# Kernel tuning notes

Hardware: AMD Instinct MI355X
Metric: run time of the kernel (lower is better)

Reference implementation:

```python
import jax, jax.numpy as jnp
import numpy as np

B, T, E, H = 2, 2048, 1024, 16
D = E // H  # head_size

def setup_inputs() -> dict:
    key = jax.random.key(0)
    ks = jax.random.split(key, 6)
    s = 0.02
    return {
        "x":  jax.random.normal(ks[0], (B, T, E), dtype=jnp.float32),
        "Wq": jax.random.normal(ks[1], (E, E), dtype=jnp.float32) * s,
        "Wk": jax.random.normal(ks[2], (E, E), dtype=jnp.float32) * s,
        "Wv": jax.random.normal(ks[3], (E, E), dtype=jnp.float32) * s,
        "Wp": jax.random.normal(ks[4], (E, E), dtype=jnp.float32) * s,
        "bp": jnp.zeros((E,), dtype=jnp.float32),
    }

def reference(x, Wq, Wk, Wv, Wp, bp):
    b, t, e = x.shape
    # Per-head Linear(E, D, bias=False) stacked == single [E,E] matmul then head split.
    # torch Linear: y = x @ W.T
    q = (x @ Wq.T).reshape(b, t, H, D).transpose(0, 2, 1, 3)  # (B,H,T,D)
    k = (x @ Wk.T).reshape(b, t, H, D).transpose(0, 2, 1, 3)
    v = (x @ Wv.T).reshape(b, t, H, D).transpose(0, 2, 1, 3)
    scale = jnp.asarray(D, x.dtype) ** -0.5
    wei = jnp.einsum('bhqd,bhkd->bhqk', q, k) * scale  # (B,H,T,T)
    causal = jnp.tril(jnp.ones((t, t), dtype=bool))
    wei = jnp.where(causal, wei, -jnp.inf)
    wei = jax.nn.softmax(wei, axis=-1)
    # dropout p=0.0 -> identity (eval-mode determinism)
    out = jnp.einsum('bhqk,bhkd->bhqd', wei, v)  # (B,H,T,D)
    out = out.transpose(0, 2, 1, 3).reshape(b, t, e)  # concat heads
    return out @ Wp.T + bp
```

## Files before the change

kernel.cpp:

```cpp
#include <hip/hip_runtime.h>

#define T_ 2048
#define E_ 1024
#define H_ 16
#define D_ 64
#define M_ 4096

typedef unsigned short ushort_t;
typedef __attribute__((ext_vector_type(8))) short bf16x8;
typedef __attribute__((ext_vector_type(4))) float f32x4;
typedef __attribute__((ext_vector_type(4))) unsigned short u16x4;
typedef __attribute__((ext_vector_type(8))) unsigned short u16x8;
typedef __attribute__((ext_vector_type(2))) unsigned int u32x2;

__device__ __forceinline__ ushort_t f2bf(float f) {
  union { float f; unsigned u; } v; v.f = f;
  unsigned r = v.u + 0x7FFFu + ((v.u >> 16) & 1u);
  return (ushort_t)(r >> 16);
}

__device__ __forceinline__ void gl16(const void* g, void* l) {
  __builtin_amdgcn_global_load_lds((const __attribute__((address_space(1))) void*)g,
                                   (__attribute__((address_space(3))) void*)l, 16, 0, 0);
}

__global__ __launch_bounds__(256)
void conv_all(const float* __restrict__ x,  const float* __restrict__ wq,
              const float* __restrict__ wk, const float* __restrict__ wv,
              const float* __restrict__ wp,
              ushort_t* __restrict__ xb,  ushort_t* __restrict__ wqb,
              ushort_t* __restrict__ wkb, ushort_t* __restrict__ wvb,
              ushort_t* __restrict__ wpb)
{
  const int id = blockIdx.x;
  const float* s; ushort_t* d; size_t off;
  if (id < 2048) { s = x; d = xb; off = (size_t)id * 2048; }
  else {
    int wsel = (id - 2048) >> 9, wid = (id - 2048) & 511;
    off = (size_t)wid * 2048;
    s = wsel == 0 ? wq : wsel == 1 ? wk : wsel == 2 ? wv : wp;
    d = wsel == 0 ? wqb : wsel == 1 ? wkb : wsel == 2 ? wvb : wpb;
  }
  size_t i = off + (size_t)threadIdx.x * 8;
  float4 a = *(const float4*)(s + i);
  float4 b = *(const float4*)(s + i + 4);
  u16x8 o;
  o[0]=f2bf(a.x); o[1]=f2bf(a.y); o[2]=f2bf(a.z); o[3]=f2bf(a.w);
  o[4]=f2bf(b.x); o[5]=f2bf(b.y); o[6]=f2bf(b.z); o[7]=f2bf(b.w);
  *(u16x8*)(d + i) = o;
}

__device__ __forceinline__ void gemm_core(const ushort_t* __restrict__ A,
                                          const ushort_t* __restrict__ W,
                                          int m0, int n0,
                                          ushort_t* As, ushort_t* Bs,
                                          f32x4 acc[4][4])
{
  const int t = threadIdx.x;
  const int lane = t & 63, w = t >> 6;
  const int g = lane >> 4, lq = lane & 15;
  const int wr = w >> 1, wc = w & 1;
  const int r0 = t >> 2;
  const int c0 = t & 3;
  const int ca0 = c0 ^ ((r0 >> 1) & 3);
  const int r1 = r0 + 64;
  const int ca1 = c0 ^ ((r1 >> 1) & 3);

  #pragma unroll
  for (int i = 0; i < 4; ++i)
    #pragma unroll
    for (int j = 0; j < 4; ++j) acc[i][j] = (f32x4){0.f,0.f,0.f,0.f};

  gl16(A + (size_t)(m0 + r0) * 1024 + ca0 * 8, As + t * 8);
  gl16(A + (size_t)(m0 + r1) * 1024 + ca1 * 8, As + 2048 + t * 8);
  gl16(W + (size_t)(n0 + r0) * 1024 + ca0 * 8, Bs + t * 8);
  gl16(W + (size_t)(n0 + r1) * 1024 + ca1 * 8, Bs + 2048 + t * 8);
  __syncthreads();

  int cur = 0;
  for (int k0 = 0; k0 < 1024; k0 += 32) {
    if (k0 + 32 < 1024) {
      const int nx = (cur ^ 1) * 4096;
      gl16(A + (size_t)(m0 + r0) * 1024 + k0 + 32 + ca0 * 8, As + nx + t * 8);
      gl16(A + (size_t)(m0 + r1) * 1024 + k0 + 32 + ca1 * 8, As + nx + 2048 + t * 8);
      gl16(W + (size_t)(n0 + r0) * 1024 + k0 + 32 + ca0 * 8, Bs + nx + t * 8);
      gl16(W + (size_t)(n0 + r1) * 1024 + k0 + 32 + ca1 * 8, Bs + nx + 2048 + t * 8);
    }
    const ushort_t* as = As + cur * 4096;
    const ushort_t* bs = Bs + cur * 4096;

    bf16x8 af[4], bfr[4];
    #pragma unroll
    for (int mi = 0; mi < 4; ++mi) {
      int row = wr * 64 + mi * 16 + lq;
      int ch = g ^ ((row >> 1) & 3);
      af[mi] = *(const bf16x8*)(as + row * 32 + ch * 8);
    }
    #pragma unroll
    for (int ni = 0; ni < 4; ++ni) {
      int row = wc * 64 + ni * 16 + lq;
      int ch = g ^ ((row >> 1) & 3);
      bfr[ni] = *(const bf16x8*)(bs + row * 32 + ch * 8);
    }
    __builtin_amdgcn_s_setprio(1);
    #pragma unroll
    for (int mi = 0; mi < 4; ++mi)
      #pragma unroll
      for (int ni = 0; ni < 4; ++ni)
        acc[mi][ni] = __builtin_amdgcn_mfma_f32_16x16x32_bf16(af[mi], bfr[ni], acc[mi][ni], 0, 0, 0);
    __builtin_amdgcn_s_setprio(0);

    __syncthreads();
    cur ^= 1;
  }
}

__global__ __launch_bounds__(256)
void gemm_qkv(const ushort_t* __restrict__ xb,
              const ushort_t* __restrict__ wqb, const ushort_t* __restrict__ wkb,
              const ushort_t* __restrict__ wvb,
              ushort_t* __restrict__ Qd, ushort_t* __restrict__ Kd, ushort_t* __restrict__ Vd)
{
  __shared__ __align__(16) ushort_t As[2 * 4096];
  __shared__ __align__(16) ushort_t Bs[2 * 4096];
  const int bx = blockIdx.x;
  const int sel = bx >> 3;
  const int n0 = (bx & 7) * 128;
  const int m0 = blockIdx.y * 128;
  const ushort_t* W = sel == 0 ? wqb : (sel == 1 ? wkb : wvb);
  f32x4 acc[4][4];
  gemm_core(xb, W, m0, n0, As, Bs, acc);

  const int t = threadIdx.x, lane = t & 63, w = t >> 6;
  const int g = lane >> 4, lq = lane & 15, wr = w >> 1, wc = w & 1;
  const float scl = (sel == 0) ? 0.125f : 1.0f;
  ushort_t* dst = sel == 0 ? Qd : (sel == 1 ? Kd : Vd);
  #pragma unroll
  for (int mi = 0; mi < 4; ++mi)
    #pragma unroll
    for (int ni = 0; ni < 4; ++ni)
      #pragma unroll
      for (int r = 0; r < 4; ++r) {
        int m = m0 + wr * 64 + mi * 16 + 4 * g + r;
        int n = n0 + wc * 64 + ni * 16 + lq;
        int b = m >> 11, tt = m & (T_ - 1);
        int h = n >> 6, d = n & (D_ - 1);
        ushort_t v = f2bf(acc[mi][ni][r] * scl);
        if (sel < 2) dst[((size_t)(b * H_ + h) * T_ + tt) * D_ + d] = v;
        else         dst[((size_t)(b * H_ + h) * D_ + d) * T_ + tt] = v;
      }
}

__global__ __launch_bounds__(256)
void gemm_out64(const ushort_t* __restrict__ Ab, const ushort_t* __restrict__ wpb,
                const float* __restrict__ bias, float* __restrict__ out)
{
  __shared__ __align__(16) ushort_t As[2 * 2048];
  __shared__ __align__(16) ushort_t Bs[2 * 4096];
  const int t = threadIdx.x, lane = t & 63, w = t >> 6;
  const int g = lane >> 4, lq = lane & 15;
  const int n0 = blockIdx.x * 128;
  const int m0 = blockIdx.y * 64;
  const int r0 = t >> 2, c0 = t & 3;
  const int ca0 = c0 ^ ((r0 >> 1) & 3);
  const int r1 = r0 + 64;
  const int ca1 = c0 ^ ((r1 >> 1) & 3);

  f32x4 acc[4][2];
  #pragma unroll
  for (int i = 0; i < 4; ++i) { acc[i][0] = (f32x4){0.f,0.f,0.f,0.f}; acc[i][1] = (f32x4){0.f,0.f,0.f,0.f}; }

  gl16(Ab  + (size_t)(m0 + r0) * 1024 + ca0 * 8, As + t * 8);
  gl16(wpb + (size_t)(n0 + r0) * 1024 + ca0 * 8, Bs + t * 8);
  gl16(wpb + (size_t)(n0 + r1) * 1024 + ca1 * 8, Bs + 2048 + t * 8);
  __syncthreads();

  int cur = 0;
  for (int k0 = 0; k0 < 1024; k0 += 32) {
    if (k0 + 32 < 1024) {
      gl16(Ab  + (size_t)(m0 + r0) * 1024 + k0 + 32 + ca0 * 8, As + (cur ^ 1) * 2048 + t * 8);
      gl16(wpb + (size_t)(n0 + r0) * 1024 + k0 + 32 + ca0 * 8, Bs + (cur ^ 1) * 4096 + t * 8);
      gl16(wpb + (size_t)(n0 + r1) * 1024 + k0 + 32 + ca1 * 8, Bs + (cur ^ 1) * 4096 + 2048 + t * 8);
    }
    const ushort_t* as = As + cur * 2048;
    const ushort_t* bs = Bs + cur * 4096;

    bf16x8 af[4], bfr[2];
    #pragma unroll
    for (int mi = 0; mi < 4; ++mi) {
      int row = mi * 16 + lq;
      int ch = g ^ ((row >> 1) & 3);
      af[mi] = *(const bf16x8*)(as + row * 32 + ch * 8);
    }
    #pragma unroll
    for (int ni = 0; ni < 2; ++ni) {
      int row = w * 32 + ni * 16 + lq;
      int ch = g ^ ((row >> 1) & 3);
      bfr[ni] = *(const bf16x8*)(bs + row * 32 + ch * 8);
    }
    __builtin_amdgcn_s_setprio(1);
    #pragma unroll
    for (int mi = 0; mi < 4; ++mi)
      #pragma unroll
      for (int ni = 0; ni < 2; ++ni)
        acc[mi][ni] = __builtin_amdgcn_mfma_f32_16x16x32_bf16(af[mi], bfr[ni], acc[mi][ni], 0, 0, 0);
    __builtin_amdgcn_s_setprio(0);

    __syncthreads();
    cur ^= 1;
  }
  #pragma unroll
  for (int mi = 0; mi < 4; ++mi)
    #pragma unroll
    for (int ni = 0; ni < 2; ++ni)
      #pragma unroll
      for (int r = 0; r < 4; ++r) {
        int m = m0 + mi * 16 + 4 * g + r;
        int n = n0 + w * 32 + ni * 16 + lq;
        out[(size_t)m * E_ + n] = acc[mi][ni][r] + bias[n];
      }
}

__global__ __launch_bounds__(256, 2)
void attn_mfma(const ushort_t* __restrict__ Q, const ushort_t* __restrict__ K,
               const ushort_t* __restrict__ Vt, ushort_t* __restrict__ O)
{
  __shared__ __align__(16) ushort_t Ps[128 * 72];
  const int t = threadIdx.x, w = t >> 6, lane = t & 63;
  const int g = lane >> 4, lq = lane & 15;
  const int i = blockIdx.x;
  const int xcd = i & 7, chunk = i >> 3;
  const int bh = xcd * 4 + (chunk >> 4);
  const int qt = (chunk < 32) ? (chunk & 15) : (15 - (chunk & 15));
  const int q0 = qt * 128;
  const size_t qkbase = (size_t)bh * T_ * D_;
  const size_t vbase  = (size_t)bh * D_ * T_;

  const int rowA = 32 * w + lq, rowB = rowA + 16;
  const int qgA = q0 + rowA, qgB = q0 + rowB;
  const bf16x8 qA0 = *(const bf16x8*)(Q + qkbase + (size_t)qgA * D_ + g * 8);
  const bf16x8 qA1 = *(const bf16x8*)(Q + qkbase + (size_t)qgA * D_ + 32 + g * 8);
  const bf16x8 qB0 = *(const bf16x8*)(Q + qkbase + (size_t)qgB * D_ + g * 8);
  const bf16x8 qB1 = *(const bf16x8*)(Q + qkbase + (size_t)qgB * D_ + 32 + g * 8);

  f32x4 accA[4], accB[4];
  #pragma unroll
  for (int db = 0; db < 4; ++db) { accA[db] = (f32x4){0.f,0.f,0.f,0.f}; accB[db] = (f32x4){0.f,0.f,0.f,0.f}; }
  float mA = -1e30f, lA = 0.f, mB = -1e30f, lB = 0.f;

  const int nt = 2 * qt + 2;

  for (int kt = 0; kt < nt; ++kt) {
    const int k0 = kt * 64;

    bf16x8 kf0[4], kf1[4], vf0[4], vf1[4];
    #pragma unroll
    for (int kb = 0; kb < 4; ++kb) {
      const ushort_t* kp = K + qkbase + (size_t)(k0 + kb * 16 + lq) * D_;
      kf0[kb] = *(const bf16x8*)(kp + g * 8);
      kf1[kb] = *(const bf16x8*)(kp + 32 + g * 8);
    }
    #pragma unroll
    for (int db = 0; db < 4; ++db) {
      const ushort_t* vp = Vt + vbase + (size_t)(db * 16 + lq) * T_ + k0;
      vf0[db] = *(const bf16x8*)(vp + g * 8);
      vf1[db] = *(const bf16x8*)(vp + 32 + g * 8);
    }

    f32x4 stA[4], stB[4];
    __builtin_amdgcn_s_setprio(1);
    #pragma unroll
    for (int kb = 0; kb < 4; ++kb) {
      f32x4 zA = (f32x4){0.f,0.f,0.f,0.f};
      zA = __builtin_amdgcn_mfma_f32_16x16x32_bf16(kf0[kb], qA0, zA, 0, 0, 0);
      zA = __builtin_amdgcn_mfma_f32_16x16x32_bf16(kf1[kb], qA1, zA, 0, 0, 0);
      stA[kb] = zA;
      f32x4 zB = (f32x4){0.f,0.f,0.f,0.f};
      zB = __builtin_amdgcn_mfma_f32_16x16x32_bf16(kf0[kb], qB0, zB, 0, 0, 0);
      zB = __builtin_amdgcn_mfma_f32_16x16x32_bf16(kf1[kb], qB1, zB, 0, 0, 0);
      stB[kb] = zB;
    }
    __builtin_amdgcn_s_setprio(0);

    if (kt >= nt - 2) {
      #pragma unroll
      for (int kb = 0; kb < 4; ++kb)
        #pragma unroll
        for (int r = 0; r < 4; ++r) {
          int kg = k0 + kb * 16 + 4 * g + r;
          if (kg > qgA) stA[kb][r] = -1e30f;
          if (kg > qgB) stB[kb][r] = -1e30f;
        }
    }

    float tmA = -1e30f, tmB = -1e30f;
    #pragma unroll
    for (int kb = 0; kb < 4; ++kb)
      #pragma unroll
      for (int r = 0; r < 4; ++r) { tmA = fmaxf(tmA, stA[kb][r]); tmB = fmaxf(tmB, stB[kb][r]); }
    tmA = fmaxf(tmA, __shfl_xor(tmA, 16)); tmA = fmaxf(tmA, __shfl_xor(tmA, 32));
    tmB = fmaxf(tmB, __shfl_xor(tmB, 16)); tmB = fmaxf(tmB, __shfl_xor(tmB, 32));

    if (!__all((tmA <= mA + 8.f) && (tmB <= mB + 8.f))) {
      float mnA = fmaxf(mA, tmA), mnB = fmaxf(mB, tmB);
      float alA = __expf(mA - mnA), alB = __expf(mB - mnB);
      mA = mnA; mB = mnB;
      lA *= alA; lB *= alB;
      float alAr[4], alBr[4];
      #pragma unroll
      for (int r = 0; r < 4; ++r) { alAr[r] = __shfl(alA, 4 * g + r); alBr[r] = __shfl(alB, 4 * g + r); }
      #pragma unroll
      for (int db = 0; db < 4; ++db)
        #pragma unroll
        for (int r = 0; r < 4; ++r) { accA[db][r] *= alAr[r]; accB[db][r] *= alBr[r]; }
    }

    float tsA = 0.f, tsB = 0.f;
    #pragma unroll
    for (int kb = 0; kb < 4; ++kb) {
      float pA0 = __expf(stA[kb][0] - mA), pA1 = __expf(stA[kb][1] - mA);
      float pA2 = __expf(stA[kb][2] - mA), pA3 = __expf(stA[kb][3] - mA);
      float pB0 = __expf(stB[kb][0] - mB), pB1 = __expf(stB[kb][1] - mB);
      float pB2 = __expf(stB[kb][2] - mB), pB3 = __expf(stB[kb][3] - mB);
      tsA += (pA0 + pA1) + (pA2 + pA3);
      tsB += (pB0 + pB1) + (pB2 + pB3);
      unsigned aLo, aHi, bLo, bHi;
      asm("v_cvt_pk_bf16_f32 %0, %1, %2" : "=v"(aLo) : "v"(pA0), "v"(pA1));
      asm("v_cvt_pk_bf16_f32 %0, %1, %2" : "=v"(aHi) : "v"(pA2), "v"(pA3));
      asm("v_cvt_pk_bf16_f32 %0, %1, %2" : "=v"(bLo) : "v"(pB0), "v"(pB1));
      asm("v_cvt_pk_bf16_f32 %0, %1, %2" : "=v"(bHi) : "v"(pB2), "v"(pB3));
      *(u32x2*)(Ps + rowA * 72 + kb * 16 + 4 * g) = (u32x2){aLo, aHi};
      *(u32x2*)(Ps + rowB * 72 + kb * 16 + 4 * g) = (u32x2){bLo, bHi};
    }
    tsA += __shfl_xor(tsA, 16); tsA += __shfl_xor(tsA, 32);
    tsB += __shfl_xor(tsB, 16); tsB += __shfl_xor(tsB, 32);
    lA += tsA; lB += tsB;

    asm volatile("s_waitcnt lgkmcnt(0)" ::: "memory");
    bf16x8 paA0 = *(const bf16x8*)(Ps + rowA * 72 + g * 8);
    bf16x8 paA1 = *(const bf16x8*)(Ps + rowA * 72 + 32 + g * 8);
    bf16x8 paB0 = *(const bf16x8*)(Ps + rowB * 72 + g * 8);
    bf16x8 paB1 = *(const bf16x8*)(Ps + rowB * 72 + 32 + g * 8);

    __builtin_amdgcn_s_setprio(1);
    #pragma unroll
    for (int db = 0; db < 4; ++db) {
      accA[db] = __builtin_amdgcn_mfma_f32_16x16x32_bf16(paA0, vf0[db], accA[db], 0, 0, 0);
      accA[db] = __builtin_amdgcn_mfma_f32_16x16x32_bf16(paA1, vf1[db], accA[db], 0, 0, 0);
      accB[db] = __builtin_amdgcn_mfma_f32_16x16x32_bf16(paB0, vf0[db], accB[db], 0, 0, 0);
      accB[db] = __builtin_amdgcn_mfma_f32_16x16x32_bf16(paB1, vf1[db], accB[db], 0, 0, 0);
    }
    __builtin_amdgcn_s_setprio(0);
  }

  float invA = 1.0f / lA, invB = 1.0f / lB;
  float liA[4], liB[4];
  #pragma unroll
  for (int r = 0; r < 4; ++r) { liA[r] = __shfl(invA, 4 * g + r); liB[r] = __shfl(invB, 4 * g + r); }
  const int b = bh >> 4, h = bh & 15;
  #pragma unroll
  for (int db = 0; db < 4; ++db)
    #pragma unroll
    for (int r = 0; r < 4; ++r) {
      int mAo = q0 + 32 * w + 4 * g + r;
      int mBo = mAo + 16;
      O[((size_t)(b * T_ + mAo)) * E_ + h * 64 + db * 16 + lq] = f2bf(accA[db][r] * liA[r]);
      O[((size_t)(b * T_ + mBo)) * E_ + h * 64 + db * 16 + lq] = f2bf(accB[db][r] * liB[r]);
    }
}

extern "C" void kernel_launch(void* const* d_in, const int* in_sizes, int n_in,
                              void* d_out, int out_size, void* d_ws, size_t ws_size,
                              hipStream_t stream) {
  const float* x  = (const float*)d_in[0];
  const float* Wq = (const float*)d_in[1];
  const float* Wk = (const float*)d_in[2];
  const float* Wv = (const float*)d_in[3];
  const float* Wp = (const float*)d_in[4];
  const float* bp = (const float*)d_in[5];
  float* out = (float*)d_out;

  ushort_t* ws  = (ushort_t*)d_ws;
  ushort_t* xb  = ws;
  ushort_t* wqb = xb  + (size_t)M_ * E_;
  ushort_t* wkb = wqb + (size_t)E_ * E_;
  ushort_t* wvb = wkb + (size_t)E_ * E_;
  ushort_t* wpb = wvb + (size_t)E_ * E_;
  ushort_t* Qb  = wpb + (size_t)E_ * E_;
  ushort_t* Kb  = Qb  + (size_t)M_ * E_;
  ushort_t* Vb  = Kb  + (size_t)M_ * E_;
  ushort_t* Ab  = Vb  + (size_t)M_ * E_;

  conv_all<<<4096, 256, 0, stream>>>(x, Wq, Wk, Wv, Wp, xb, wqb, wkb, wvb, wpb);
  gemm_qkv<<<dim3(24, 32), 256, 0, stream>>>(xb, wqb, wkb, wvb, Qb, Kb, Vb);
  attn_mfma<<<512, 256, 0, stream>>>(Qb, Kb, Vb, Ab);
  gemm_out64<<<dim3(8, 64), 256, 0, stream>>>(Ab, wpb, bp, out);
}
```

Measured before the change: 135.1 us.

## Software-pipeline K tile loads with double-buffered registers in attention loop

Unrolls the key-tile loop by two and double-buffers K fragments in registers, so the next tile's K is prefetched while the current tile's softmax and PV work run. V loads are issued after the QK MFMAs so they overlap the softmax arithmetic. The aim is to hide global load latency behind compute, at the cost of higher register pressure that could lower occupancy or cause spills.

```diff
diff --git a/kernel.cpp b/kernel.cpp
--- a/kernel.cpp
+++ b/kernel.cpp
@@ -9,7 +9,6 @@
 typedef unsigned short ushort_t;
 typedef __attribute__((ext_vector_type(8))) short bf16x8;
 typedef __attribute__((ext_vector_type(4))) float f32x4;
-typedef __attribute__((ext_vector_type(4))) unsigned short u16x4;
 typedef __attribute__((ext_vector_type(8))) unsigned short u16x8;
 typedef __attribute__((ext_vector_type(2))) unsigned int u32x2;
 
@@ -250,108 +249,129 @@
 
   const int nt = 2 * qt + 2;
 
-  for (int kt = 0; kt < nt; ++kt) {
-    const int k0 = kt * 64;
-
-    bf16x8 kf0[4], kf1[4], vf0[4], vf1[4];
-    #pragma unroll
-    for (int kb = 0; kb < 4; ++kb) {
-      const ushort_t* kp = K + qkbase + (size_t)(k0 + kb * 16 + lq) * D_;
-      kf0[kb] = *(const bf16x8*)(kp + g * 8);
-      kf1[kb] = *(const bf16x8*)(kp + 32 + g * 8);
-    }
-    #pragma unroll
-    for (int db = 0; db < 4; ++db) {
-      const ushort_t* vp = Vt + vbase + (size_t)(db * 16 + lq) * T_ + k0;
-      vf0[db] = *(const bf16x8*)(vp + g * 8);
-      vf1[db] = *(const bf16x8*)(vp + 32 + g * 8);
-    }
-
-    f32x4 stA[4], stB[4];
-    __builtin_amdgcn_s_setprio(1);
-    #pragma unroll
-    for (int kb = 0; kb < 4; ++kb) {
-      f32x4 zA = (f32x4){0.f,0.f,0.f,0.f};
-      zA = __builtin_amdgcn_mfma_f32_16x16x32_bf16(kf0[kb], qA0, zA, 0, 0, 0);
-      zA = __builtin_amdgcn_mfma_f32_16x16x32_bf16(kf1[kb], qA1, zA, 0, 0, 0);
-      stA[kb] = zA;
-      f32x4 zB = (f32x4){0.f,0.f,0.f,0.f};
-      zB = __builtin_amdgcn_mfma_f32_16x16x32_bf16(kf0[kb], qB0, zB, 0, 0, 0);
-      zB = __builtin_amdgcn_mfma_f32_16x16x32_bf16(kf1[kb], qB1, zB, 0, 0, 0);
-      stB[kb] = zB;
-    }
-    __builtin_amdgcn_s_setprio(0);
-
-    if (kt >= nt - 2) {
-      #pragma unroll
-      for (int kb = 0; kb < 4; ++kb)
-        #pragma unroll
-        for (int r = 0; r < 4; ++r) {
-          int kg = k0 + kb * 16 + 4 * g + r;
-          if (kg > qgA) stA[kb][r] = -1e30f;
-          if (kg > qgB) stB[kb][r] = -1e30f;
-        }
-    }
-
-    float tmA = -1e30f, tmB = -1e30f;
-    #pragma unroll
-    for (int kb = 0; kb < 4; ++kb)
-      #pragma unroll
-      for (int r = 0; r < 4; ++r) { tmA = fmaxf(tmA, stA[kb][r]); tmB = fmaxf(tmB, stB[kb][r]); }
-    tmA = fmaxf(tmA, __shfl_xor(tmA, 16)); tmA = fmaxf(tmA, __shfl_xor(tmA, 32));
-    tmB = fmaxf(tmB, __shfl_xor(tmB, 16)); tmB = fmaxf(tmB, __shfl_xor(tmB, 32));
-
-    if (!__all((tmA <= mA + 8.f) && (tmB <= mB + 8.f))) {
-      float mnA = fmaxf(mA, tmA), mnB = fmaxf(mB, tmB);
-      float alA = __expf(mA - mnA), alB = __expf(mB - mnB);
-      mA = mnA; mB = mnB;
-      lA *= alA; lB *= alB;
-      float alAr[4], alBr[4];
-      #pragma unroll
-      for (int r = 0; r < 4; ++r) { alAr[r] = __shfl(alA, 4 * g + r); alBr[r] = __shfl(alB, 4 * g + r); }
-      #pragma unroll
-      for (int db = 0; db < 4; ++db)
-        #pragma unroll
-        for (int r = 0; r < 4; ++r) { accA[db][r] *= alAr[r]; accB[db][r] *= alBr[r]; }
-    }
-
-    float tsA = 0.f, tsB = 0.f;
-    #pragma unroll
-    for (int kb = 0; kb < 4; ++kb) {
-      float pA0 = __expf(stA[kb][0] - mA), pA1 = __expf(stA[kb][1] - mA);
-      float pA2 = __expf(stA[kb][2] - mA), pA3 = __expf(stA[kb][3] - mA);
-      float pB0 = __expf(stB[kb][0] - mB), pB1 = __expf(stB[kb][1] - mB);
-      float pB2 = __expf(stB[kb][2] - mB), pB3 = __expf(stB[kb][3] - mB);
-      tsA += (pA0 + pA1) + (pA2 + pA3);
-      tsB += (pB0 + pB1) + (pB2 + pB3);
-      unsigned aLo, aHi, bLo, bHi;
-      asm("v_cvt_pk_bf16_f32 %0, %1, %2" : "=v"(aLo) : "v"(pA0), "v"(pA1));
-      asm("v_cvt_pk_bf16_f32 %0, %1, %2" : "=v"(aHi) : "v"(pA2), "v"(pA3));
-      asm("v_cvt_pk_bf16_f32 %0, %1, %2" : "=v"(bLo) : "v"(pB0), "v"(pB1));
-      asm("v_cvt_pk_bf16_f32 %0, %1, %2" : "=v"(bHi) : "v"(pB2), "v"(pB3));
-      *(u32x2*)(Ps + rowA * 72 + kb * 16 + 4 * g) = (u32x2){aLo, aHi};
-      *(u32x2*)(Ps + rowB * 72 + kb * 16 + 4 * g) = (u32x2){bLo, bHi};
-    }
-    tsA += __shfl_xor(tsA, 16); tsA += __shfl_xor(tsA, 32);
-    tsB += __shfl_xor(tsB, 16); tsB += __shfl_xor(tsB, 32);
-    lA += tsA; lB += tsB;
-
-    asm volatile("s_waitcnt lgkmcnt(0)" ::: "memory");
-    bf16x8 paA0 = *(const bf16x8*)(Ps + rowA * 72 + g * 8);
-    bf16x8 paA1 = *(const bf16x8*)(Ps + rowA * 72 + 32 + g * 8);
-    bf16x8 paB0 = *(const bf16x8*)(Ps + rowB * 72 + g * 8);
-    bf16x8 paB1 = *(const bf16x8*)(Ps + rowB * 72 + 32 + g * 8);
-
-    __builtin_amdgcn_s_setprio(1);
-    #pragma unroll
-    for (int db = 0; db < 4; ++db) {
-      accA[db] = __builtin_amdgcn_mfma_f32_16x16x32_bf16(paA0, vf0[db], accA[db], 0, 0, 0);
-      accA[db] = __builtin_amdgcn_mfma_f32_16x16x32_bf16(paA1, vf1[db], accA[db], 0, 0, 0);
-      accB[db] = __builtin_amdgcn_mfma_f32_16x16x32_bf16(paB0, vf0[db], accB[db], 0, 0, 0);
-      accB[db] = __builtin_amdgcn_mfma_f32_16x16x32_bf16(paB1, vf1[db], accB[db], 0, 0, 0);
-    }
-    __builtin_amdgcn_s_setprio(0);
+  bf16x8 kfa0[4], kfa1[4], kfb0[4], kfb1[4];
+  bf16x8 vf0[4], vf1[4];
+
+#define LOADK(K0_, KF0_, KF1_)                                                \
+  do {                                                                        \
+    _Pragma("unroll")                                                         \
+    for (int _i = 0; _i < 4; ++_i) {                                          \
+      const ushort_t* _kp = K + qkbase + (size_t)((K0_) + _i * 16 + lq) * D_; \
+      KF0_[_i] = *(const bf16x8*)(_kp + g * 8);                               \
+      KF1_[_i] = *(const bf16x8*)(_kp + 32 + g * 8);                          \
+    }                                                                         \
+  } while (0)
+
+#define LOADV(K0_)                                                              \
+  do {                                                                          \
+    _Pragma("unroll")                                                           \
+    for (int _i = 0; _i < 4; ++_i) {                                            \
+      const ushort_t* _vp = Vt + vbase + (size_t)(_i * 16 + lq) * T_ + (K0_);   \
+      vf0[_i] = *(const bf16x8*)(_vp + g * 8);                                  \
+      vf1[_i] = *(const bf16x8*)(_vp + 32 + g * 8);                             \
+    }                                                                           \
+  } while (0)
+
+#define STEP(K0_, KF0_, KF1_, KN0_, NKF0_, NKF1_, DOMASK)                       \
+  do {                                                                          \
+    const int _k0 = (K0_);                                                      \
+    f32x4 stA[4], stB[4];                                                       \
+    __builtin_amdgcn_s_setprio(1);                                              \
+    _Pragma("unroll")                                                           \
+    for (int _kb = 0; _kb < 4; ++_kb) {                                         \
+      f32x4 zA = (f32x4){0.f,0.f,0.f,0.f};                                      \
+      zA = __builtin_amdgcn_mfma_f32_16x16x32_bf16(KF0_[_kb], qA0, zA, 0, 0, 0);\
+      zA = __builtin_amdgcn_mfma_f32_16x16x32_bf16(KF1_[_kb], qA1, zA, 0, 0, 0);\
+      stA[_kb] = zA;                                                            \
+      f32x4 zB = (f32x4){0.f,0.f,0.f,0.f};                                      \
+      zB = __builtin_amdgcn_mfma_f32_16x16x32_bf16(KF0_[_kb], qB0, zB, 0, 0, 0);\
+      zB = __builtin_amdgcn_mfma_f32_16x16x32_bf16(KF1_[_kb], qB1, zB, 0, 0, 0);\
+      stB[_kb] = zB;                                                            \
+    }                                                                           \
+    __builtin_amdgcn_s_setprio(0);                                              \
+    LOADV(_k0);                          \
+    if ((KN0_) >= 0) LOADK((KN0_), NKF0_, NKF1_);          \
+    if (DOMASK) {                                                               \
+      _Pragma("unroll")                                                         \
+      for (int _kb = 0; _kb < 4; ++_kb)                                         \
+        _Pragma("unroll")                                                       \
+        for (int _r = 0; _r < 4; ++_r) {                                        \
+          int _kg = _k0 + _kb * 16 + 4 * g + _r;                                \
+          if (_kg > qgA) stA[_kb][_r] = -1e30f;                                 \
+          if (_kg > qgB) stB[_kb][_r] = -1e30f;                                 \
+        }                                                                       \
+    }                                                                           \
+    float tmA = -1e30f, tmB = -1e30f;                                           \
+    _Pragma("unroll")                                                           \
+    for (int _kb = 0; _kb < 4; ++_kb)                                           \
+      _Pragma("unroll")                                                         \
+      for (int _r = 0; _r < 4; ++_r) {                                          \
+        tmA = fmaxf(tmA, stA[_kb][_r]); tmB = fmaxf(tmB, stB[_kb][_r]);         \
+      }                                                                         \
+    tmA = fmaxf(tmA, __shfl_xor(tmA, 16)); tmA = fmaxf(tmA, __shfl_xor(tmA, 32));\
+    tmB = fmaxf(tmB, __shfl_xor(tmB, 16)); tmB = fmaxf(tmB, __shfl_xor(tmB, 32));\
+    if (!__all((tmA <= mA + 8.f) && (tmB <= mB + 8.f))) {                       \
+      float mnA = fmaxf(mA, tmA), mnB = fmaxf(mB, tmB);                         \
+      float alA = __expf(mA - mnA), alB = __expf(mB - mnB);                     \
+      mA = mnA; mB = mnB;                                                       \
+      lA *= alA; lB *= alB;                                                     \
+      float alAr[4], alBr[4];                                                   \
+      _Pragma("unroll")                                                         \
+      for (int _r = 0; _r < 4; ++_r) {                                          \
+        alAr[_r] = __shfl(alA, 4 * g + _r); alBr[_r] = __shfl(alB, 4 * g + _r); \
+      }                                                                         \
+      _Pragma("unroll")                                                         \
+      for (int _db = 0; _db < 4; ++_db)                                         \
+        _Pragma("unroll")                                                       \
+        for (int _r = 0; _r < 4; ++_r) {                                        \
+          accA[_db][_r] *= alAr[_r]; accB[_db][_r] *= alBr[_r];                 \
+        }                                                                       \
+    }                                                                           \
+    float tsA = 0.f, tsB = 0.f;                                                 \
+    _Pragma("unroll")                                                           \
+    for (int _kb = 0; _kb < 4; ++_kb) {                                         \
+      float pA0 = __expf(stA[_kb][0] - mA), pA1 = __expf(stA[_kb][1] - mA);     \
+      float pA2 = __expf(stA[_kb][2] - mA), pA3 = __expf(stA[_kb][3] - mA);     \
+      float pB0 = __expf(stB[_kb][0] - mB), pB1 = __expf(stB[_kb][1] - mB);     \
+      float pB2 = __expf(stB[_kb][2] - mB), pB3 = __expf(stB[_kb][3] - mB);     \
+      tsA += (pA0 + pA1) + (pA2 + pA3);                                         \
+      tsB += (pB0 + pB1) + (pB2 + pB3);                                         \
+      unsigned aLo, aHi, bLo, bHi;                                              \
+      asm("v_cvt_pk_bf16_f32 %0, %1, %2" : "=v"(aLo) : "v"(pA0), "v"(pA1));     \
+      asm("v_cvt_pk_bf16_f32 %0, %1, %2" : "=v"(aHi) : "v"(pA2), "v"(pA3));     \
+      asm("v_cvt_pk_bf16_f32 %0, %1, %2" : "=v"(bLo) : "v"(pB0), "v"(pB1));     \
+      asm("v_cvt_pk_bf16_f32 %0, %1, %2" : "=v"(bHi) : "v"(pB2), "v"(pB3));     \
+      *(u32x2*)(Ps + rowA * 72 + _kb * 16 + 4 * g) = (u32x2){aLo, aHi};         \
+      *(u32x2*)(Ps + rowB * 72 + _kb * 16 + 4 * g) = (u32x2){bLo, bHi};         \
+    }                                                                           \
+    tsA += __shfl_xor(tsA, 16); tsA += __shfl_xor(tsA, 32);                     \
+    tsB += __shfl_xor(tsB, 16); tsB += __shfl_xor(tsB, 32);                     \
+    lA += tsA; lB += tsB;                                                       \
+    asm volatile("s_waitcnt lgkmcnt(0)" ::: "memory");                          \
+    bf16x8 paA0 = *(const bf16x8*)(Ps + rowA * 72 + g * 8);                     \
+    bf16x8 paA1 = *(const bf16x8*)(Ps + rowA * 72 + 32 + g * 8);                \
+    bf16x8 paB0 = *(const bf16x8*)(Ps + rowB * 72 + g * 8);                     \
+    bf16x8 paB1 = *(const bf16x8*)(Ps + rowB * 72 + 32 + g * 8);                \
+    __builtin_amdgcn_s_setprio(1);                                              \
+    _Pragma("unroll")                                                           \
+    for (int _db = 0; _db < 4; ++_db) {                                         \
+      accA[_db] = __builtin_amdgcn_mfma_f32_16x16x32_bf16(paA0, vf0[_db], accA[_db], 0, 0, 0); \
+      accA[_db] = __builtin_amdgcn_mfma_f32_16x16x32_bf16(paA1, vf1[_db], accA[_db], 0, 0, 0); \
+      accB[_db] = __builtin_amdgcn_mfma_f32_16x16x32_bf16(paB0, vf0[_db], accB[_db], 0, 0, 0); \
+      accB[_db] = __builtin_amdgcn_mfma_f32_16x16x32_bf16(paB1, vf1[_db], accB[_db], 0, 0, 0); \
+    }                                                                           \
+    __builtin_amdgcn_s_setprio(0);                                              \
+  } while (0)
+
+  LOADK(0, kfa0, kfa1);
+  for (int kt = 0; kt < nt; kt += 2) {
+    const bool last = (kt == nt - 2);
+    STEP(kt * 64,       kfa0, kfa1, (kt + 1) * 64,                       kfb0, kfb1, last);
+    STEP((kt + 1) * 64, kfb0, kfb1, (kt + 2 < nt) ? (kt + 2) * 64 : -1,  kfa0, kfa1, last);
   }
+#undef LOADK
+#undef LOADV
+#undef STEP
 
   float invA = 1.0f / lA, invB = 1.0f / lB;
   float liA[4], liB[4];
```

After: 135.7 us. No clear change (+0.4%).

## Halve attention query tile to 64 rows and double grid with longest-first ordering

Applied to the files above, without the earlier changes.

The attention kernel now gives each block 64 query rows (one 16-row tile per wave) instead of 128 (two per wave), which doubles the grid to 1024 blocks and raises the launch-bounds occupancy hint to 4 blocks per CU. The block order changes from an XCD-aware swizzle with paired query tiles to a simple longest-first order across (batch, head). The intent is better load balance over the causal triangle, less register pressure and more waves in flight. In exchange each loaded K/V tile feeds half as many query rows, so global and L2 traffic for K and V roughly doubles, and the XCD cache locality of the old mapping is lost.

```diff
diff --git a/kernel.cpp b/kernel.cpp
--- a/kernel.cpp
+++ b/kernel.cpp
@@ -9,7 +9,6 @@
 typedef unsigned short ushort_t;
 typedef __attribute__((ext_vector_type(8))) short bf16x8;
 typedef __attribute__((ext_vector_type(4))) float f32x4;
-typedef __attribute__((ext_vector_type(4))) unsigned short u16x4;
 typedef __attribute__((ext_vector_type(8))) unsigned short u16x8;
 typedef __attribute__((ext_vector_type(2))) unsigned int u32x2;
 
@@ -221,34 +220,31 @@
       }
 }
 
-__global__ __launch_bounds__(256, 2)
+__global__ __launch_bounds__(256, 4)
 void attn_mfma(const ushort_t* __restrict__ Q, const ushort_t* __restrict__ K,
                const ushort_t* __restrict__ Vt, ushort_t* __restrict__ O)
 {
-  __shared__ __align__(16) ushort_t Ps[128 * 72];
+  __shared__ __align__(16) ushort_t Ps[64 * 72];
   const int t = threadIdx.x, w = t >> 6, lane = t & 63;
   const int g = lane >> 4, lq = lane & 15;
   const int i = blockIdx.x;
-  const int xcd = i & 7, chunk = i >> 3;
-  const int bh = xcd * 4 + (chunk >> 4);
-  const int qt = (chunk < 32) ? (chunk & 15) : (15 - (chunk & 15));
-  const int q0 = qt * 128;
+  const int qt = 31 - (i >> 5);
+  const int bh = i & 31;
+  const int q0 = qt * 64;
   const size_t qkbase = (size_t)bh * T_ * D_;
   const size_t vbase  = (size_t)bh * D_ * T_;
 
-  const int rowA = 32 * w + lq, rowB = rowA + 16;
-  const int qgA = q0 + rowA, qgB = q0 + rowB;
+  const int rowA = 16 * w + lq;
+  const int qgA = q0 + rowA;
   const bf16x8 qA0 = *(const bf16x8*)(Q + qkbase + (size_t)qgA * D_ + g * 8);
   const bf16x8 qA1 = *(const bf16x8*)(Q + qkbase + (size_t)qgA * D_ + 32 + g * 8);
-  const bf16x8 qB0 = *(const bf16x8*)(Q + qkbase + (size_t)qgB * D_ + g * 8);
-  const bf16x8 qB1 = *(const bf16x8*)(Q + qkbase + (size_t)qgB * D_ + 32 + g * 8);
-
-  f32x4 accA[4], accB[4];
-  #pragma unroll
-  for (int db = 0; db < 4; ++db) { accA[db] = (f32x4){0.f,0.f,0.f,0.f}; accB[db] = (f32x4){0.f,0.f,0.f,0.f}; }
-  float mA = -1e30f, lA = 0.f, mB = -1e30f, lB = 0.f;
-
-  const int nt = 2 * qt + 2;
+
+  f32x4 acc[4];
+  #pragma unroll
+  for (int db = 0; db < 4; ++db) acc[db] = (f32x4){0.f,0.f,0.f,0.f};
+  float mA = -1e30f, lA = 0.f;
+
+  const int nt = qt + 1;
 
   for (int kt = 0; kt < nt; ++kt) {
     const int k0 = kt * 64;
@@ -267,105 +263,88 @@
       vf1[db] = *(const bf16x8*)(vp + 32 + g * 8);
     }
 
-    f32x4 stA[4], stB[4];
+    f32x4 st[4];
     __builtin_amdgcn_s_setprio(1);
     #pragma unroll
     for (int kb = 0; kb < 4; ++kb) {
-      f32x4 zA = (f32x4){0.f,0.f,0.f,0.f};
-      zA = __builtin_amdgcn_mfma_f32_16x16x32_bf16(kf0[kb], qA0, zA, 0, 0, 0);
-      zA = __builtin_amdgcn_mfma_f32_16x16x32_bf16(kf1[kb], qA1, zA, 0, 0, 0);
-      stA[kb] = zA;
-      f32x4 zB = (f32x4){0.f,0.f,0.f,0.f};
-      zB = __builtin_amdgcn_mfma_f32_16x16x32_bf16(kf0[kb], qB0, zB, 0, 0, 0);
-      zB = __builtin_amdgcn_mfma_f32_16x16x32_bf16(kf1[kb], qB1, zB, 0, 0, 0);
-      stB[kb] = zB;
+      f32x4 z = (f32x4){0.f,0.f,0.f,0.f};
+      z = __builtin_amdgcn_mfma_f32_16x16x32_bf16(kf0[kb], qA0, z, 0, 0, 0);
+      z = __builtin_amdgcn_mfma_f32_16x16x32_bf16(kf1[kb], qA1, z, 0, 0, 0);
+      st[kb] = z;
     }
     __builtin_amdgcn_s_setprio(0);
 
-    if (kt >= nt - 2) {
+    if (kt == nt - 1) {
       #pragma unroll
       for (int kb = 0; kb < 4; ++kb)
         #pragma unroll
         for (int r = 0; r < 4; ++r) {
           int kg = k0 + kb * 16 + 4 * g + r;
-          if (kg > qgA) stA[kb][r] = -1e30f;
-          if (kg > qgB) stB[kb][r] = -1e30f;
+          if (kg > qgA) st[kb][r] = -1e30f;
         }
     }
 
-    float tmA = -1e30f, tmB = -1e30f;
+    float tm = -1e30f;
     #pragma unroll
     for (int kb = 0; kb < 4; ++kb)
       #pragma unroll
-      for (int r = 0; r < 4; ++r) { tmA = fmaxf(tmA, stA[kb][r]); tmB = fmaxf(tmB, stB[kb][r]); }
-    tmA = fmaxf(tmA, __shfl_xor(tmA, 16)); tmA = fmaxf(tmA, __shfl_xor(tmA, 32));
-    tmB = fmaxf(tmB, __shfl_xor(tmB, 16)); tmB = fmaxf(tmB, __shfl_xor(tmB, 32));
-
-    if (!__all((tmA <= mA + 8.f) && (tmB <= mB + 8.f))) {
-      float mnA = fmaxf(mA, tmA), mnB = fmaxf(mB, tmB);
-      float alA = __expf(mA - mnA), alB = __expf(mB - mnB);
-      mA = mnA; mB = mnB;
-      lA *= alA; lB *= alB;
-      float alAr[4], alBr[4];
-      #pragma unroll
-      for (int r = 0; r < 4; ++r) { alAr[r] = __shfl(alA, 4 * g + r); alBr[r] = __shfl(alB, 4 * g + r); }
+      for (int r = 0; r < 4; ++r) tm = fmaxf(tm, st[kb][r]);
+    tm = fmaxf(tm, __shfl_xor(tm, 16));
+    tm = fmaxf(tm, __shfl_xor(tm, 32));
+
+    if (!__all(tm <= mA + 8.f)) {
+      float mn = fmaxf(mA, tm);
+      float al = __expf(mA - mn);
+      mA = mn;
+      lA *= al;
+      float alr[4];
+      #pragma unroll
+      for (int r = 0; r < 4; ++r) alr[r] = __shfl(al, 4 * g + r);
       #pragma unroll
       for (int db = 0; db < 4; ++db)
         #pragma unroll
-        for (int r = 0; r < 4; ++r) { accA[db][r] *= alAr[r]; accB[db][r] *= alBr[r]; }
-    }
-
-    float tsA = 0.f, tsB = 0.f;
+        for (int r = 0; r < 4; ++r) acc[db][r] *= alr[r];
+    }
+
+    float ts = 0.f;
     #pragma unroll
     for (int kb = 0; kb < 4; ++kb) {
-      float pA0 = __expf(stA[kb][0] - mA), pA1 = __expf(stA[kb][1] - mA);
-      float pA2 = __expf(stA[kb][2] - mA), pA3 = __expf(stA[kb][3] - mA);
-      float pB0 = __expf(stB[kb][0] - mB), pB1 = __expf(stB[kb][1] - mB);
-      float pB2 = __expf(stB[kb][2] - mB), pB3 = __expf(stB[kb][3] - mB);
-      tsA += (pA0 + pA1) + (pA2 + pA3);
-      tsB += (pB0 + pB1) + (pB2 + pB3);
-      unsigned aLo, aHi, bLo, bHi;
-      asm("v_cvt_pk_bf16_f32 %0, %1, %2" : "=v"(aLo) : "v"(pA0), "v"(pA1));
-      asm("v_cvt_pk_bf16_f32 %0, %1, %2" : "=v"(aHi) : "v"(pA2), "v"(pA3));
-      asm("v_cvt_pk_bf16_f32 %0, %1, %2" : "=v"(bLo) : "v"(pB0), "v"(pB1));
-      asm("v_cvt_pk_bf16_f32 %0, %1, %2" : "=v"(bHi) : "v"(pB2), "v"(pB3));
-      *(u32x2*)(Ps + rowA * 72 + kb * 16 + 4 * g) = (u32x2){aLo, aHi};
-      *(u32x2*)(Ps + rowB * 72 + kb * 16 + 4 * g) = (u32x2){bLo, bHi};
-    }
-    tsA += __shfl_xor(tsA, 16); tsA += __shfl_xor(tsA, 32);
-    tsB += __shfl_xor(tsB, 16); tsB += __shfl_xor(tsB, 32);
-    lA += tsA; lB += tsB;
+      float p0 = __expf(st[kb][0] - mA), p1 = __expf(st[kb][1] - mA);
+      float p2 = __expf(st[kb][2] - mA), p3 = __expf(st[kb][3] - mA);
+      ts += (p0 + p1) + (p2 + p3);
+      unsigned lo, hi;
+      asm("v_cvt_pk_bf16_f32 %0, %1, %2" : "=v"(lo) : "v"(p0), "v"(p1));
+      asm("v_cvt_pk_bf16_f32 %0, %1, %2" : "=v"(hi) : "v"(p2), "v"(p3));
+      *(u32x2*)(Ps + rowA * 72 + kb * 16 + 4 * g) = (u32x2){lo, hi};
+    }
+    ts += __shfl_xor(ts, 16);
+    ts += __shfl_xor(ts, 32);
+    lA += ts;
 
     asm volatile("s_waitcnt lgkmcnt(0)" ::: "memory");
-    bf16x8 paA0 = *(const bf16x8*)(Ps + rowA * 72 + g * 8);
-    bf16x8 paA1 = *(const bf16x8*)(Ps + rowA * 72 + 32 + g * 8);
-    bf16x8 paB0 = *(const bf16x8*)(Ps + rowB * 72 + g * 8);
-    bf16x8 paB1 = *(const bf16x8*)(Ps + rowB * 72 + 32 + g * 8);
+    bf16x8 pa0 = *(const bf16x8*)(Ps + rowA * 72 + g * 8);
+    bf16x8 pa1 = *(const bf16x8*)(Ps + rowA * 72 + 32 + g * 8);
 
     __builtin_amdgcn_s_setprio(1);
     #pragma unroll
     for (int db = 0; db < 4; ++db) {
-      accA[db] = __builtin_amdgcn_mfma_f32_16x16x32_bf16(paA0, vf0[db], accA[db], 0, 0, 0);
-      accA[db] = __builtin_amdgcn_mfma_f32_16x16x32_bf16(paA1, vf1[db], accA[db], 0, 0, 0);
-      accB[db] = __builtin_amdgcn_mfma_f32_16x16x32_bf16(paB0, vf0[db], accB[db], 0, 0, 0);
-      accB[db] = __builtin_amdgcn_mfma_f32_16x16x32_bf16(paB1, vf1[db], accB[db], 0, 0, 0);
+      acc[db] = __builtin_amdgcn_mfma_f32_16x16x32_bf16(pa0, vf0[db], acc[db], 0, 0, 0);
+      acc[db] = __builtin_amdgcn_mfma_f32_16x16x32_bf16(pa1, vf1[db], acc[db], 0, 0, 0);
     }
     __builtin_amdgcn_s_setprio(0);
   }
 
-  float invA = 1.0f / lA, invB = 1.0f / lB;
-  float liA[4], liB[4];
-  #pragma unroll
-  for (int r = 0; r < 4; ++r) { liA[r] = __shfl(invA, 4 * g + r); liB[r] = __shfl(invB, 4 * g + r); }
+  float inv = 1.0f / lA;
+  float li[4];
+  #pragma unroll
+  for (int r = 0; r < 4; ++r) li[r] = __shfl(inv, 4 * g + r);
   const int b = bh >> 4, h = bh & 15;
   #pragma unroll
   for (int db = 0; db < 4; ++db)
     #pragma unroll
     for (int r = 0; r < 4; ++r) {
-      int mAo = q0 + 32 * w + 4 * g + r;
-      int mBo = mAo + 16;
-      O[((size_t)(b * T_ + mAo)) * E_ + h * 64 + db * 16 + lq] = f2bf(accA[db][r] * liA[r]);
-      O[((size_t)(b * T_ + mBo)) * E_ + h * 64 + db * 16 + lq] = f2bf(accB[db][r] * liB[r]);
+      int mo = q0 + 16 * w + 4 * g + r;
+      O[((size_t)(b * T_ + mo)) * E_ + h * 64 + db * 16 + lq] = f2bf(acc[db][r] * li[r]);
     }
 }
 
@@ -393,6 +372,6 @@
 
   conv_all<<<4096, 256, 0, stream>>>(x, Wq, Wk, Wv, Wp, xb, wqb, wkb, wvb, wpb);
   gemm_qkv<<<dim3(24, 32), 256, 0, stream>>>(xb, wqb, wkb, wvb, Qb, Kb, Vb);
-  attn_mfma<<<512, 256, 0, stream>>>(Qb, Kb, Vb, Ab);
+  attn_mfma<<<1024, 256, 0, stream>>>(Qb, Kb, Vb, Ab);
   gemm_out64<<<dim3(8, 64), 256, 0, stream>>>(Ab, wpb, bp, out);
 }
```

Result: slower. 213.1 us (+57.7%).

## Split long causal attention query tiles across two blocks and merge partials

Applied to the files above, without the earlier changes.

Query tiles 8-15 now have their key range split into two halves, each handled by its own block that writes unnormalized fp32 partial outputs plus row max and sum. A new merge kernel combines the two halves with log-sum-exp rescaling and writes bf16 output. Short tiles still run in a single block, and longest-first ordering is meant to even out the causal load imbalance and tail. Launch bounds also go up to 3 blocks per SM. The cost is an extra kernel launch, fp32 partial traffic through workspace, and reuse of the xb buffer for the max/sum scratch, which is safe only because xb is no longer read after the QKV GEMM.

```diff
diff --git a/kernel.cpp b/kernel.cpp
--- a/kernel.cpp
+++ b/kernel.cpp
@@ -9,7 +9,6 @@
 typedef unsigned short ushort_t;
 typedef __attribute__((ext_vector_type(8))) short bf16x8;
 typedef __attribute__((ext_vector_type(4))) float f32x4;
-typedef __attribute__((ext_vector_type(4))) unsigned short u16x4;
 typedef __attribute__((ext_vector_type(8))) unsigned short u16x8;
 typedef __attribute__((ext_vector_type(2))) unsigned int u32x2;
 
@@ -221,17 +220,31 @@
       }
 }
 
-__global__ __launch_bounds__(256, 2)
+__global__ __launch_bounds__(256, 3)
 void attn_mfma(const ushort_t* __restrict__ Q, const ushort_t* __restrict__ K,
-               const ushort_t* __restrict__ Vt, ushort_t* __restrict__ O)
+               const ushort_t* __restrict__ Vt, ushort_t* __restrict__ O,
+               float* __restrict__ Op, float* __restrict__ Mp, float* __restrict__ Lp)
 {
   __shared__ __align__(16) ushort_t Ps[128 * 72];
   const int t = threadIdx.x, w = t >> 6, lane = t & 63;
   const int g = lane >> 4, lq = lane & 15;
-  const int i = blockIdx.x;
-  const int xcd = i & 7, chunk = i >> 3;
-  const int bh = xcd * 4 + (chunk >> 4);
-  const int qt = (chunk < 32) ? (chunk & 15) : (15 - (chunk & 15));
+  const int j = blockIdx.x;
+  int qt, bh, ks, ke;
+  bool split;
+  if (j < 512) {
+    split = true;
+    qt = 15 - (j >> 6);
+    int s = (j >> 5) & 1;
+    bh = j & 31;
+    ks = s * (qt + 1);
+    ke = ks + qt + 1;
+  } else {
+    split = false;
+    qt = 7 - ((j - 512) >> 5);
+    bh = (j - 512) & 31;
+    ks = 0;
+    ke = 2 * qt + 2;
+  }
   const int q0 = qt * 128;
   const size_t qkbase = (size_t)bh * T_ * D_;
   const size_t vbase  = (size_t)bh * D_ * T_;
@@ -248,9 +261,7 @@
   for (int db = 0; db < 4; ++db) { accA[db] = (f32x4){0.f,0.f,0.f,0.f}; accB[db] = (f32x4){0.f,0.f,0.f,0.f}; }
   float mA = -1e30f, lA = 0.f, mB = -1e30f, lB = 0.f;
 
-  const int nt = 2 * qt + 2;
-
-  for (int kt = 0; kt < nt; ++kt) {
+  for (int kt = ks; kt < ke; ++kt) {
     const int k0 = kt * 64;
 
     bf16x8 kf0[4], kf1[4], vf0[4], vf1[4];
@@ -282,7 +293,7 @@
     }
     __builtin_amdgcn_s_setprio(0);
 
-    if (kt >= nt - 2) {
+    if (kt >= 2 * qt) {
       #pragma unroll
       for (int kb = 0; kb < 4; ++kb)
         #pragma unroll
@@ -353,20 +364,73 @@
     __builtin_amdgcn_s_setprio(0);
   }
 
-  float invA = 1.0f / lA, invB = 1.0f / lB;
-  float liA[4], liB[4];
-  #pragma unroll
-  for (int r = 0; r < 4; ++r) { liA[r] = __shfl(invA, 4 * g + r); liB[r] = __shfl(invB, 4 * g + r); }
+  if (split) {
+    float* op = Op + (size_t)j * 128 * 64;
+    #pragma unroll
+    for (int db = 0; db < 4; ++db)
+      #pragma unroll
+      for (int r = 0; r < 4; ++r) {
+        int rA = 32 * w + 4 * g + r;
+        op[rA * 64 + db * 16 + lq] = accA[db][r];
+        op[(rA + 16) * 64 + db * 16 + lq] = accB[db][r];
+      }
+    if (g == 0) {
+      Mp[j * 128 + rowA] = mA;  Lp[j * 128 + rowA] = lA;
+      Mp[j * 128 + rowB] = mB;  Lp[j * 128 + rowB] = lB;
+    }
+  } else {
+    float invA = 1.0f / lA, invB = 1.0f / lB;
+    float liA[4], liB[4];
+    #pragma unroll
+    for (int r = 0; r < 4; ++r) { liA[r] = __shfl(invA, 4 * g + r); liB[r] = __shfl(invB, 4 * g + r); }
+    const int b = bh >> 4, h = bh & 15;
+    #pragma unroll
+    for (int db = 0; db < 4; ++db)
+      #pragma unroll
+      for (int r = 0; r < 4; ++r) {
+        int mAo = q0 + 32 * w + 4 * g + r;
+        int mBo = mAo + 16;
+        O[((size_t)(b * T_ + mAo)) * E_ + h * 64 + db * 16 + lq] = f2bf(accA[db][r] * liA[r]);
+        O[((size_t)(b * T_ + mBo)) * E_ + h * 64 + db * 16 + lq] = f2bf(accB[db][r] * liB[r]);
+      }
+  }
+}
+
+__global__ __launch_bounds__(256)
+void merge_attn(const float* __restrict__ Op, const float* __restrict__ Mp,
+                const float* __restrict__ Lp, ushort_t* __restrict__ O)
+{
+  const int mb = blockIdx.x;
+  const int grp = mb >> 5;
+  const int qt = 15 - grp;
+  const int bh = mb & 31;
+  const int j0 = grp * 64 + bh;
+  const int j1 = j0 + 32;
+  const int q0 = qt * 128;
   const int b = bh >> 4, h = bh & 15;
-  #pragma unroll
-  for (int db = 0; db < 4; ++db)
-    #pragma unroll
-    for (int r = 0; r < 4; ++r) {
-      int mAo = q0 + 32 * w + 4 * g + r;
-      int mBo = mAo + 16;
-      O[((size_t)(b * T_ + mAo)) * E_ + h * 64 + db * 16 + lq] = f2bf(accA[db][r] * liA[r]);
-      O[((size_t)(b * T_ + mBo)) * E_ + h * 64 + db * 16 + lq] = f2bf(accB[db][r] * liB[r]);
-    }
+
+  const int tid = threadIdx.x;
+  const int row = tid >> 1;
+  const int ch = (tid & 1) * 32;
+
+  const float m0 = Mp[j0 * 128 + row], l0 = Lp[j0 * 128 + row];
+  const float m1 = Mp[j1 * 128 + row], l1 = Lp[j1 * 128 + row];
+  const float m = fmaxf(m0, m1);
+  const float c0 = __expf(m0 - m), c1 = __expf(m1 - m);
+  const float inv = 1.0f / (l0 * c0 + l1 * c1);
+
+  const float* p0 = Op + (size_t)j0 * 128 * 64 + row * 64 + ch;
+  const float* p1 = Op + (size_t)j1 * 128 * 64 + row * 64 + ch;
+  ushort_t* dst = O + ((size_t)(b * T_ + q0 + row)) * E_ + h * 64 + ch;
+  #pragma unroll
+  for (int c = 0; c < 32; c += 4) {
+    float4 a0 = *(const float4*)(p0 + c);
+    float4 a1 = *(const float4*)(p1 + c);
+    dst[c + 0] = f2bf((a0.x * c0 + a1.x * c1) * inv);
+    dst[c + 1] = f2bf((a0.y * c0 + a1.y * c1) * inv);
+    dst[c + 2] = f2bf((a0.z * c0 + a1.z * c1) * inv);
+    dst[c + 3] = f2bf((a0.w * c0 + a1.w * c1) * inv);
+  }
 }
 
 extern "C" void kernel_launch(void* const* d_in, const int* in_sizes, int n_in,
@@ -390,9 +454,13 @@
   ushort_t* Kb  = Qb  + (size_t)M_ * E_;
   ushort_t* Vb  = Kb  + (size_t)M_ * E_;
   ushort_t* Ab  = Vb  + (size_t)M_ * E_;
+  float* Op = (float*)(Ab + (size_t)M_ * E_);
+  float* Mp = (float*)xb;
+  float* Lp = Mp + 512 * 128;
 
   conv_all<<<4096, 256, 0, stream>>>(x, Wq, Wk, Wv, Wp, xb, wqb, wkb, wvb, wpb);
   gemm_qkv<<<dim3(24, 32), 256, 0, stream>>>(xb, wqb, wkb, wvb, Qb, Kb, Vb);
-  attn_mfma<<<512, 256, 0, stream>>>(Qb, Kb, Vb, Ab);
+  attn_mfma<<<768, 256, 0, stream>>>(Qb, Kb, Vb, Ab, Op, Mp, Lp);
+  merge_attn<<<256, 256, 0, stream>>>(Op, Mp, Lp, Ab);
   gemm_out64<<<dim3(8, 64), 256, 0, stream>>>(Ab, wpb, bp, out);
 }
```

Result: slower. 160.5 us (+18.8%).
